# Optimization experiments

Hardware: AMD Instinct MI355X
Metric: run time of the kernel (lower is better)

The kernel has to match this reference:

```python
import jax, jax.numpy as jnp
import numpy as np

N = 8192        # nodes
IN_F = 256      # in_features
OUT_F = 64      # out_features per head
HEADS = 4
ALPHA = 0.2     # leaky relu slope
NEG_INF = -9e15


def setup_inputs() -> dict:
    key = jax.random.key(0)
    ks = jax.random.split(key, 8)
    h = jax.random.normal(ks[0], (N, IN_F), dtype=jnp.float32)
    adj = jax.random.randint(ks[1], (N, N), 0, 2, dtype=jnp.int32)
    # per-head GAT params, stacked over heads
    W = jax.random.normal(ks[2], (HEADS, IN_F, OUT_F), dtype=jnp.float32) * (1.0 / np.sqrt(IN_F))
    a1 = jax.random.normal(ks[3], (HEADS, OUT_F), dtype=jnp.float32) * (1.0 / np.sqrt(OUT_F))
    a2 = jax.random.normal(ks[4], (HEADS, OUT_F), dtype=jnp.float32) * (1.0 / np.sqrt(OUT_F))
    # fusing linear: Linear(out*heads, out)
    fc_w = jax.random.normal(ks[5], (OUT_F, HEADS * OUT_F), dtype=jnp.float32) * (1.0 / np.sqrt(HEADS * OUT_F))
    fc_b = jax.random.normal(ks[6], (OUT_F,), dtype=jnp.float32) * 0.01
    return {"h": h, "adj": adj, "W": W, "a1": a1, "a2": a2, "fc_w": fc_w, "fc_b": fc_b}


def reference(h, adj, W, a1, a2, fc_w, fc_b):
    # all heads batched: Wh [H, N, F]
    Wh = jnp.einsum('ni,hio->hno', h, W)
    # attention logits e_ij = leakyrelu(a1.Wh_i + a2.Wh_j), shape [H, N, N]
    e_src = jnp.einsum('hno,ho->hn', Wh, a1)   # [H, N]
    e_dst = jnp.einsum('hno,ho->hn', Wh, a2)   # [H, N]
    e = jax.nn.leaky_relu(e_src[:, :, None] + e_dst[:, None, :], ALPHA)
    e = jnp.where(adj[None] > 0, e, NEG_INF)
    attn = jax.nn.softmax(e, axis=-1)          # masked softmax over neighbors
    out = jnp.einsum('hnm,hmo->hno', attn, Wh)  # [H, N, F]
    out = jax.nn.elu(out)
    # concat heads along feature dim -> [N, H*F], then fuse linear
    h_concat = jnp.transpose(out, (1, 0, 2)).reshape(N, HEADS * OUT_F)
    return h_concat @ fc_w.T + fc_b
```

## Files before the change

### kernel.cpp

```cpp
#include <hip/hip_runtime.h>
#include <hip/hip_bf16.h>

#define NN 8192
#define NHEADS 4
#define OUTF 64
#define NCHUNK 4
#define CHUNK 2048
#define ROWS 32
#define LOG2E 1.4426950408889634f

typedef __bf16 bf16x8 __attribute__((ext_vector_type(8)));
typedef float fx4 __attribute__((ext_vector_type(4)));
typedef unsigned short ushort8 __attribute__((ext_vector_type(8)));

__global__ __launch_bounds__(256) void k_wh(
    const float* __restrict__ h, const float* __restrict__ W,
    const float* __restrict__ a1, const float* __restrict__ a2,
    unsigned short* __restrict__ whsw, float* __restrict__ R,
    float* __restrict__ F1, float* __restrict__ F2)
{
  __shared__ float ws[64 * 260];
  const int tid = threadIdx.x;
  const int hd = blockIdx.x >> 7;
  const int i0 = (blockIdx.x & 127) << 6;

  const float* Wp = W + hd * (256 * 64);
  for (int idx = tid; idx < 256 * 64; idx += 256) {
    int k = idx >> 6, o = idx & 63;
    ws[o * 260 + k] = Wp[idx];
  }
  __syncthreads();

  const int w = tid >> 6, o = tid & 63;
  const int ibase = i0 + w * 16;
  float acc[16];
#pragma unroll
  for (int m = 0; m < 16; ++m) acc[m] = 0.f;

  const float* hp = h + (size_t)ibase * 256;
  for (int k4 = 0; k4 < 64; ++k4) {
    fx4 wv = *(const fx4*)(&ws[o * 260 + k4 * 4]);
#pragma unroll
    for (int m = 0; m < 16; ++m) {
      fx4 hv = *(const fx4*)(hp + m * 256 + k4 * 4);
      acc[m] += hv[0] * wv[0] + hv[1] * wv[1] + hv[2] * wv[2] + hv[3] * wv[3];
    }
  }

  const float a1v = a1[hd * 64 + o], a2v = a2[hd * 64 + o];
#pragma unroll
  for (int m = 0; m < 16; ++m) {
    float s1 = acc[m] * a1v, s2 = acc[m] * a2v;
#pragma unroll
    for (int d = 1; d < 64; d <<= 1) {
      s1 += __shfl_xor(s1, d);
      s2 += __shfl_xor(s2, d);
    }
    if (o == 0) {
      int ix = hd * NN + ibase + m;
      R[ix]  = __builtin_amdgcn_exp2f(-0.8f * s1 * LOG2E);
      F1[ix] = __builtin_amdgcn_exp2f(s2 * LOG2E);
      F2[ix] = __builtin_amdgcn_exp2f(0.2f * s2 * LOG2E);
    }
  }

  size_t base = (size_t)hd * 524288 + (size_t)((i0 >> 5) + (w >> 1)) * 2048 +
                (size_t)(o >> 4) * 512;
  int ln0 = (o & 15) + 16 * ((w & 1) * 2);
  ushort8 pk0, pk1;
#pragma unroll
  for (int m = 0; m < 8; ++m) {
    pk0[m] = __builtin_bit_cast(unsigned short, (__bf16)acc[m]);
    pk1[m] = __builtin_bit_cast(unsigned short, (__bf16)acc[m + 8]);
  }
  *(ushort8*)(whsw + base + (size_t)ln0 * 8) = pk0;
  *(ushort8*)(whsw + base + (size_t)(ln0 + 16) * 8) = pk1;
}

struct Tile {
  fx4 f1a, f1b, f2a, f2b;
  bf16x8 b0, b1, b2, b3;
  unsigned m0, m1;
};

__device__ __forceinline__ void load_tile(Tile& t, const float* F1p,
                                          const float* F2p,
                                          const unsigned short* wp,
                                          const unsigned* bm, int il, int jb)
{
  t.f1a = *(const fx4*)(F1p + jb);
  t.f1b = *(const fx4*)(F1p + jb + 4);
  t.f2a = *(const fx4*)(F2p + jb);
  t.f2b = *(const fx4*)(F2p + jb + 4);
  const unsigned short* wq = wp + (size_t)(jb >> 5) * 2048;
  t.b0 = *(const bf16x8*)(wq);
  t.b1 = *(const bf16x8*)(wq + 512);
  t.b2 = *(const bf16x8*)(wq + 1024);
  t.b3 = *(const bf16x8*)(wq + 1536);
  const unsigned* mb = bm + (jb >> 5) * ROWS;
  t.m0 = mb[il];
  t.m1 = mb[16 + il];
}

__device__ __forceinline__ void compute_tile(const Tile& t, const float* Rr,
                                             int g, const bf16x8& ones,
                                             fx4 acc[2][4], fx4* accS)
{
#pragma unroll
  for (int rs = 0; rs < 2; ++rs) {
    unsigned sm = (rs ? t.m1 : t.m0) >> (g * 8);
    float p[8];
#pragma unroll
    for (int e = 0; e < 8; ++e) {
      float f1 = (e < 4) ? t.f1a[e] : t.f1b[e - 4];
      float f2 = (e < 4) ? t.f2a[e] : t.f2b[e - 4];
      float pm = fmaxf(f1, Rr[rs] * f2);
      unsigned keep = (unsigned)(((int)(sm << (31 - e))) >> 31);
      p[e] = __builtin_bit_cast(float,
                 __builtin_bit_cast(unsigned, pm) & keep);
    }
    bf16x8 af;
#pragma unroll
    for (int e = 0; e < 8; ++e) af[e] = (__bf16)p[e];
    acc[rs][0] = __builtin_amdgcn_mfma_f32_16x16x32_bf16(af, t.b0, acc[rs][0], 0, 0, 0);
    acc[rs][1] = __builtin_amdgcn_mfma_f32_16x16x32_bf16(af, t.b1, acc[rs][1], 0, 0, 0);
    acc[rs][2] = __builtin_amdgcn_mfma_f32_16x16x32_bf16(af, t.b2, acc[rs][2], 0, 0, 0);
    acc[rs][3] = __builtin_amdgcn_mfma_f32_16x16x32_bf16(af, t.b3, acc[rs][3], 0, 0, 0);
    accS[rs] = __builtin_amdgcn_mfma_f32_16x16x32_bf16(af, ones, accS[rs], 0, 0, 0);
  }
}

__global__ __launch_bounds__(256) void k_attn(
    const int* __restrict__ adj, const unsigned short* __restrict__ whsw,
    const float* __restrict__ Rg, const float* __restrict__ F1g,
    const float* __restrict__ F2g, float* __restrict__ pacc,
    float* __restrict__ psum)
{
  __shared__ unsigned bm[(CHUNK / 32) * ROWS];
  const int tid = threadIdx.x;
  const int lane = tid & 63;
  const int hd = tid >> 6;
  const int ci = blockIdx.x & 3;
  const int i0 = (blockIdx.x >> 2) << 5;
  const int j0 = ci * CHUNK;
  const int il = lane & 15;
  const int g = lane >> 4;

  {
    const int wv = hd;
    for (int it = 0; it < 8; ++it) {
      int tb = wv * 256 + it * 32;
#pragma unroll 4
      for (int blk = 0; blk < 4; ++blk) {
        int v[8];
#pragma unroll
        for (int u = 0; u < 8; ++u) {
          int t = tb + blk * 8 + u;
          int row = t >> 5, sg = t & 31;
          v[u] = adj[(size_t)(i0 + row) * NN + j0 + sg * 64 + lane];
        }
#pragma unroll
        for (int u = 0; u < 8; ++u) {
          int t = tb + blk * 8 + u;
          int row = t >> 5, sg = t & 31;
          unsigned long long m = __ballot(v[u] != 0);
          unsigned word = (lane == 1) ? (unsigned)(m >> 32) : (unsigned)m;
          if (lane < 2) bm[(sg * 2 + lane) * ROWS + row] = word;
        }
      }
    }
  }
  __syncthreads();

  float Rr[2];
#pragma unroll
  for (int rs = 0; rs < 2; ++rs)
    Rr[rs] = Rg[hd * NN + i0 + rs * 16 + il];
  const float* F1p = F1g + hd * NN + j0 + g * 8;
  const float* F2p = F2g + hd * NN + j0 + g * 8;
  const unsigned short* wp = whsw + (size_t)hd * 524288 +
                             (size_t)(j0 >> 5) * 2048 + (size_t)lane * 8;
  bf16x8 ones;
#pragma unroll
  for (int e = 0; e < 8; ++e) ones[e] = (__bf16)1.0f;

  fx4 acc[2][4] = {};
  fx4 accS[2] = {};

  Tile t0, t1;
  load_tile(t0, F1p, F2p, wp, bm, il, 0);
  for (int jb = 0; jb < CHUNK; jb += 64) {
    load_tile(t1, F1p, F2p, wp, bm, il, jb + 32);
    compute_tile(t0, Rr, g, ones, acc, accS);
    if (jb + 64 < CHUNK) load_tile(t0, F1p, F2p, wp, bm, il, jb + 64);
    compute_tile(t1, Rr, g, ones, acc, accS);
  }

#pragma unroll
  for (int rs = 0; rs < 2; ++rs) {
    if (il == 0) {
#pragma unroll
      for (int r = 0; r < 4; ++r)
        psum[(size_t)(ci * NHEADS + hd) * NN + i0 + rs * 16 + g * 4 + r] =
            accS[rs][r];
    }
  }

  float* pc = pacc + (size_t)ci * NN * 256;
#pragma unroll
  for (int rs = 0; rs < 2; ++rs)
#pragma unroll
    for (int r = 0; r < 4; ++r)
#pragma unroll
      for (int ft = 0; ft < 4; ++ft)
        pc[(size_t)(i0 + rs * 16 + g * 4 + r) * 256 + hd * 64 + ft * 16 + il] =
            acc[rs][ft][r];
}

__global__ __launch_bounds__(256) void k_fc(
    const float* __restrict__ pacc, const float* __restrict__ psum,
    const float* __restrict__ fcw, const float* __restrict__ fcb,
    float* __restrict__ out)
{
  __shared__ float ws[256 * 65];
  __shared__ float ash[32 * 260];
  __shared__ float inv[32 * 4];
  const int tid = threadIdx.x;
  const int i0 = blockIdx.x * 32;

  for (int idx = tid; idx < 64 * 256; idx += 256) {
    int o = idx >> 8, c = idx & 255;
    ws[c * 65 + o] = fcw[idx];
  }
  if (tid < 128) {
    int m = tid >> 2, hh = tid & 3;
    float s = 0.f;
#pragma unroll
    for (int ci = 0; ci < NCHUNK; ++ci)
      s += psum[(size_t)(ci * NHEADS + hh) * NN + i0 + m];
    inv[m * 4 + hh] = 1.0f / s;
  }
  __syncthreads();

  for (int idx = tid; idx < 32 * 64; idx += 256) {
    int m = idx >> 6, q = idx & 63;
    int hh = q >> 4;
    size_t off = (size_t)(i0 + m) * 256 + q * 4;
    fx4 v = {};
#pragma unroll
    for (int ci = 0; ci < NCHUNK; ++ci) {
      fx4 a = *(const fx4*)(pacc + (size_t)ci * NN * 256 + off);
      v[0] += a[0]; v[1] += a[1]; v[2] += a[2]; v[3] += a[3];
    }
    float iv = inv[m * 4 + hh];
#pragma unroll
    for (int j = 0; j < 4; ++j) {
      float x = v[j] * iv;
      x = (x > 0.f) ? x : (__builtin_amdgcn_exp2f(x * LOG2E) - 1.0f);
      ash[m * 260 + q * 4 + j] = x;
    }
  }
  __syncthreads();

  const int w = tid >> 6, o = tid & 63;
  float acc[8];
#pragma unroll
  for (int m = 0; m < 8; ++m) acc[m] = 0.f;

  for (int c4 = 0; c4 < 64; ++c4) {
    float w0 = ws[(c4 * 4 + 0) * 65 + o];
    float w1 = ws[(c4 * 4 + 1) * 65 + o];
    float w2 = ws[(c4 * 4 + 2) * 65 + o];
    float w3 = ws[(c4 * 4 + 3) * 65 + o];
#pragma unroll
    for (int m = 0; m < 8; ++m) {
      fx4 hv = *(const fx4*)(&ash[(w * 8 + m) * 260 + c4 * 4]);
      acc[m] += hv[0] * w0 + hv[1] * w1 + hv[2] * w2 + hv[3] * w3;
    }
  }
  const float bo = fcb[o];
#pragma unroll
  for (int m = 0; m < 8; ++m)
    out[(size_t)(i0 + w * 8 + m) * 64 + o] = acc[m] + bo;
}

extern "C" void kernel_launch(void* const* d_in, const int* in_sizes, int n_in,
                              void* d_out, int out_size, void* d_ws, size_t ws_size,
                              hipStream_t stream) {
  (void)in_sizes; (void)n_in; (void)out_size; (void)ws_size;
  const float* h   = (const float*)d_in[0];
  const int*   adj = (const int*)d_in[1];
  const float* W   = (const float*)d_in[2];
  const float* a1  = (const float*)d_in[3];
  const float* a2  = (const float*)d_in[4];
  const float* fcw = (const float*)d_in[5];
  const float* fcb = (const float*)d_in[6];
  float* out = (float*)d_out;

  char* base = (char*)d_ws;
  unsigned short* whsw = (unsigned short*)base;
  float* R  = (float*)(base + (4u << 20));
  float* F1 = (float*)(base + (4u << 20) + (128u << 10));
  float* F2 = (float*)(base + (4u << 20) + (256u << 10));
  float* pacc = (float*)(base + (4u << 20) + (512u << 10));
  float* psum = (float*)(base + (36u << 20) + (512u << 10));

  k_wh<<<dim3(512), dim3(256), 0, stream>>>(h, W, a1, a2, whsw, R, F1, F2);
  k_attn<<<dim3(1024), dim3(256), 0, stream>>>(adj, whsw, R, F1, F2, pacc, psum);
  k_fc<<<dim3(256), dim3(256), 0, stream>>>(pacc, psum, fcw, fcb, out);
}
```

Baseline: 225.2 us.

## Precompute adjacency bitmask in separate kernel and halve column chunks in attention

A new kernel streams the int32 adjacency matrix once and packs it into a global bitmask with wave ballots. The attention kernel then loads its slice of the compact bitmask into shared memory through an XOR-swizzled layout, instead of reading and ballot-packing raw adjacency itself. The column split drops from four chunks to two, so each block covers twice as many neighbours and fewer partial accumulators are written for the final reduction. The trade-off is an extra kernel launch and bitmask round trip through global memory, plus half as many attention blocks, which may leave the GPU less fully occupied.

New measurement: 231.6 us. 2.8% more time.

```diff
diff --git a/kernel.cpp b/kernel.cpp
--- a/kernel.cpp
+++ b/kernel.cpp
@@ -4,14 +4,36 @@
 #define NN 8192
 #define NHEADS 4
 #define OUTF 64
-#define NCHUNK 4
-#define CHUNK 2048
+#define NCHUNK 2
+#define CHUNK 4096
 #define ROWS 32
 #define LOG2E 1.4426950408889634f
 
 typedef __bf16 bf16x8 __attribute__((ext_vector_type(8)));
 typedef float fx4 __attribute__((ext_vector_type(4)));
 typedef unsigned short ushort8 __attribute__((ext_vector_type(8)));
+
+__global__ __launch_bounds__(256) void k_bits(
+    const int* __restrict__ adj, unsigned* __restrict__ bm)
+{
+  const int lane = threadIdx.x & 63;
+  const int row = blockIdx.x * 4 + (threadIdx.x >> 6);
+  const int* ap = adj + (size_t)row * NN;
+  unsigned* bp = bm + (size_t)row * (NN / 32);
+
+  for (int it8 = 0; it8 < 16; ++it8) {
+    int v[8];
+#pragma unroll
+    for (int u = 0; u < 8; ++u)
+      v[u] = ap[(it8 * 8 + u) * 64 + lane];
+#pragma unroll
+    for (int u = 0; u < 8; ++u) {
+      unsigned long long m = __ballot(v[u] != 0);
+      unsigned word = (lane == 1) ? (unsigned)(m >> 32) : (unsigned)m;
+      if (lane < 2) bp[(it8 * 8 + u) * 2 + lane] = word;
+    }
+  }
+}
 
 __global__ __launch_bounds__(256) void k_wh(
     const float* __restrict__ h, const float* __restrict__ W,
@@ -80,13 +102,13 @@
 struct Tile {
   fx4 f1a, f1b, f2a, f2b;
   bf16x8 b0, b1, b2, b3;
-  unsigned m0, m1;
+  unsigned m[2];
 };
 
 __device__ __forceinline__ void load_tile(Tile& t, const float* F1p,
                                           const float* F2p,
                                           const unsigned short* wp,
-                                          const unsigned* bm, int il, int jb)
+                                          const unsigned* bml, int il, int jb)
 {
   t.f1a = *(const fx4*)(F1p + jb);
   t.f1b = *(const fx4*)(F1p + jb + 4);
@@ -97,9 +119,9 @@
   t.b1 = *(const bf16x8*)(wq + 512);
   t.b2 = *(const bf16x8*)(wq + 1024);
   t.b3 = *(const bf16x8*)(wq + 1536);
-  const unsigned* mb = bm + (jb >> 5) * ROWS;
-  t.m0 = mb[il];
-  t.m1 = mb[16 + il];
+  const int jw = jb >> 5;
+  t.m[0] = bml[jw * 32 + (il ^ (jw & 31))];
+  t.m[1] = bml[jw * 32 + ((16 + il) ^ (jw & 31))];
 }
 
 __device__ __forceinline__ void compute_tile(const Tile& t, const float* Rr,
@@ -108,7 +130,7 @@
 {
 #pragma unroll
   for (int rs = 0; rs < 2; ++rs) {
-    unsigned sm = (rs ? t.m1 : t.m0) >> (g * 8);
+    unsigned sm = t.m[rs] >> (g * 8);
     float p[8];
 #pragma unroll
     for (int e = 0; e < 8; ++e) {
@@ -131,44 +153,27 @@
 }
 
 __global__ __launch_bounds__(256) void k_attn(
-    const int* __restrict__ adj, const unsigned short* __restrict__ whsw,
+    const unsigned* __restrict__ bm, const unsigned short* __restrict__ whsw,
     const float* __restrict__ Rg, const float* __restrict__ F1g,
     const float* __restrict__ F2g, float* __restrict__ pacc,
     float* __restrict__ psum)
 {
-  __shared__ unsigned bm[(CHUNK / 32) * ROWS];
+  __shared__ unsigned bml[(CHUNK / 32) * ROWS];
   const int tid = threadIdx.x;
   const int lane = tid & 63;
   const int hd = tid >> 6;
-  const int ci = blockIdx.x & 3;
-  const int i0 = (blockIdx.x >> 2) << 5;
+  const int bx = blockIdx.x;
+  const int ci = bx & 1;
+  const int i0 = (bx >> 1) << 5;
   const int j0 = ci * CHUNK;
   const int il = lane & 15;
   const int g = lane >> 4;
 
-  {
-    const int wv = hd;
-    for (int it = 0; it < 8; ++it) {
-      int tb = wv * 256 + it * 32;
-#pragma unroll 4
-      for (int blk = 0; blk < 4; ++blk) {
-        int v[8];
-#pragma unroll
-        for (int u = 0; u < 8; ++u) {
-          int t = tb + blk * 8 + u;
-          int row = t >> 5, sg = t & 31;
-          v[u] = adj[(size_t)(i0 + row) * NN + j0 + sg * 64 + lane];
-        }
-#pragma unroll
-        for (int u = 0; u < 8; ++u) {
-          int t = tb + blk * 8 + u;
-          int row = t >> 5, sg = t & 31;
-          unsigned long long m = __ballot(v[u] != 0);
-          unsigned word = (lane == 1) ? (unsigned)(m >> 32) : (unsigned)m;
-          if (lane < 2) bm[(sg * 2 + lane) * ROWS + row] = word;
-        }
-      }
-    }
+  for (int it = 0; it < 16; ++it) {
+    int idx = it * 256 + tid;
+    int r = idx >> 7, w = idx & 127;
+    unsigned v = bm[(size_t)(i0 + r) * (NN / 32) + (j0 >> 5) + w];
+    bml[w * 32 + (r ^ (w & 31))] = v;
   }
   __syncthreads();
 
@@ -188,11 +193,11 @@
   fx4 accS[2] = {};
 
   Tile t0, t1;
-  load_tile(t0, F1p, F2p, wp, bm, il, 0);
+  load_tile(t0, F1p, F2p, wp, bml, il, 0);
   for (int jb = 0; jb < CHUNK; jb += 64) {
-    load_tile(t1, F1p, F2p, wp, bm, il, jb + 32);
+    load_tile(t1, F1p, F2p, wp, bml, il, jb + 32);
     compute_tile(t0, Rr, g, ones, acc, accS);
-    if (jb + 64 < CHUNK) load_tile(t0, F1p, F2p, wp, bm, il, jb + 64);
+    if (jb + 64 < CHUNK) load_tile(t0, F1p, F2p, wp, bml, il, jb + 64);
     compute_tile(t1, Rr, g, ones, acc, accS);
   }
 
@@ -302,10 +307,12 @@
   float* R  = (float*)(base + (4u << 20));
   float* F1 = (float*)(base + (4u << 20) + (128u << 10));
   float* F2 = (float*)(base + (4u << 20) + (256u << 10));
-  float* pacc = (float*)(base + (4u << 20) + (512u << 10));
-  float* psum = (float*)(base + (36u << 20) + (512u << 10));
-
+  unsigned* bmask = (unsigned*)(base + (5u << 20));
+  float* pacc = (float*)(base + (13u << 20));
+  float* psum = (float*)(base + (29u << 20));
+
+  k_bits<<<dim3(2048), dim3(256), 0, stream>>>(adj, bmask);
   k_wh<<<dim3(512), dim3(256), 0, stream>>>(h, W, a1, a2, whsw, R, F1, F2);
-  k_attn<<<dim3(1024), dim3(256), 0, stream>>>(adj, whsw, R, F1, F2, pacc, psum);
+  k_attn<<<dim3(512), dim3(256), 0, stream>>>(bmask, whsw, R, F1, F2, pacc, psum);
   k_fc<<<dim3(256), dim3(256), 0, stream>>>(pacc, psum, fcw, fcb, out);
 }
```
